# Kernel optimization log

Measured on AMD Instinct MI355X. Metric: run time of the kernel, lower is better.

## Reference

```python
import jax, jax.numpy as jnp
import numpy as np

H = 1024          # rnn hidden dim
D = H // 2        # coarse/fine half
E = H // 8        # embed dim = 128
COND = H // 2     # conditioning (upsampled mel) dim = 512
EPS = 1e-5
TILE = 16


def _bn(x, scale, offset):
    # haiku BatchNorm, training mode: batch stats over (N, L)
    mean = jnp.mean(x, axis=(0, 1), keepdims=True)
    var = jnp.mean(jnp.square(x), axis=(0, 1), keepdims=True) - jnp.square(mean)
    return scale * (x - mean) * jax.lax.rsqrt(var + EPS) + offset


def _conv(x, w, rate=1):
    return jax.lax.conv_general_dilated(
        x, w, window_strides=(1,), padding='VALID', rhs_dilation=(rate,),
        dimension_numbers=('NWC', 'WIO', 'NWC'))


def _up(x, w, stride):
    # Conv1DTranspose with kernel 1, SAME padding: scatter x@w to positions i*stride
    N, L, _ = x.shape
    y = jnp.einsum('nlc,cd->nld', x, w)
    out = jnp.zeros((N, L, stride, y.shape[-1]), y.dtype).at[:, :, 0, :].set(y)
    return out.reshape(N, L * stride, y.shape[-1])


def _iw_mask():
    m = jnp.ones((COND + 3 * E, 3 * H), jnp.float32)
    for j in (0, 2, 4):  # coarse_t embed cannot see coarse half of u, r, e gates
        m = m.at[-E:, j * D:(j + 1) * D].set(0.0)
    return m


def _forward(x, mel, conv_in_w, bn0_s, bn0_o, dconv1_w, bn1_s, bn1_o,
             dconv2_w, bn2_s, bn2_o, up1_w, bn3_s, bn3_o, up2_w, bn4_s, bn4_o,
             up3_w, bn5_s, bn5_o, I_W, I_b, R_w, R_b,
             O1_w, O1_b, O2_w, O2_b, O3_w, O3_b, O4_w, O4_b, c_embed, f_embed):
    # ---- UpsampleNetwork ----
    h = jax.nn.relu(_bn(_conv(mel, conv_in_w), bn0_s, bn0_o))
    r1 = jax.nn.relu(_bn(_conv(h, dconv1_w, rate=2), bn1_s, bn1_o))
    h = h[:, 1:-1] + r1
    r2 = jax.nn.relu(_bn(_conv(h, dconv2_w, rate=4), bn2_s, bn2_o))
    h = h[:, 2:-2] + r2
    h = jax.nn.relu(_bn(_up(h, up1_w, 2), bn3_s, bn3_o))
    h = jax.nn.relu(_bn(_up(h, up2_w, 2), bn4_s, bn4_o))
    h = jax.nn.relu(_bn(_up(h, up3_w, 4), bn5_s, bn5_o))
    N, Lm, Dm = h.shape
    mel_up = jnp.tile(h[:, :, None, :], (1, 1, TILE, 1)).reshape(N, Lm * TILE, Dm)

    # ---- WaveRNNOriginal.__call__ (teacher-forced GRU) ----
    coarse, fine, coarse_t = x[..., 0], x[..., 1], x[..., 2]
    inputs = jnp.concatenate(
        (mel_up, c_embed[coarse], f_embed[fine], c_embed[coarse_t]), axis=-1)
    # precompute input projection for all timesteps  [N, L, 3H]
    ix = jnp.einsum('nli,ij->nlj', inputs, I_W * _iw_mask()) + I_b.reshape(1, 1, -1)
    ix_t = jnp.swapaxes(ix, 0, 1)  # time-major [L, N, 3H]
    h0 = jnp.zeros((N, H), ix.dtype)

    def step(hx, xt):
        u1, r1_, e1 = jnp.split(hx @ R_w + R_b, 3, axis=-1)
        u2, r2_, e2 = jnp.split(xt, 3, axis=-1)
        ut = jax.nn.sigmoid(u1 + u2)
        rt = jax.nn.sigmoid(r1_ + r2_)
        et = jnp.tanh(rt * e1 + e2)
        ht = ut * hx + (1.0 - ut) * et
        return ht, ht

    _, hs = jax.lax.scan(step, h0, ix_t)
    hs = jnp.swapaxes(hs, 0, 1)              # [N, L, H]
    yc, yf = jnp.split(hs, 2, axis=-1)       # [N, L, H/2] each
    clog = jax.nn.relu(yc @ O1_w + O1_b) @ O2_w + O2_b
    flog = jax.nn.relu(yf @ O3_w + O3_b) @ O4_w + O4_b
    logits = jnp.stack((clog, flog), axis=-1)  # [N, L, 256, 2]
    return jax.nn.log_softmax(logits, axis=-2)


def setup_inputs():
    key = jax.random.key(0)
    ks = jax.random.split(key, 24)
    n = jax.random.normal
    N, T = 2, 24
    L = (T - 8) * 256  # 4096
    inp = {
        'x': jax.random.randint(ks[0], (N, L, 3), 0, 256),
        'mel': n(ks[1], (N, T, 80), jnp.float32),
        'conv_in_w': n(ks[2], (3, 80, 512)) * 0.05,
        'dconv1_w': n(ks[3], (2, 512, 512)) * 0.05,
        'dconv2_w': n(ks[4], (2, 512, 512)) * 0.05,
        'up1_w': n(ks[5], (512, 512)) * 0.05,
        'up2_w': n(ks[6], (512, 512)) * 0.05,
        'up3_w': n(ks[7], (512, COND)) * 0.05,
        'I_W': n(ks[8], (COND + 3 * E, 3 * H)) * 0.03,
        'I_b': jnp.zeros((3 * H,)),
        'R_w': n(ks[9], (H, 3 * H)) * 0.03,
        'R_b': jnp.zeros((3 * H,)),
        'O1_w': n(ks[10], (D, D)) * 0.05,
        'O1_b': jnp.zeros((D,)),
        'O2_w': n(ks[11], (D, 256)) * 0.05,
        'O2_b': jnp.zeros((256,)),
        'O3_w': n(ks[12], (D, D)) * 0.05,
        'O3_b': jnp.zeros((D,)),
        'O4_w': n(ks[13], (D, 256)) * 0.05,
        'O4_b': jnp.zeros((256,)),
        'c_embed': n(ks[14], (256, E)) * 0.1,
        'f_embed': n(ks[15], (256, E)) * 0.1,
    }
    for i in range(6):
        c = COND if i == 5 else 512
        inp[f'bn{i}_s'] = jnp.ones((c,))
        inp[f'bn{i}_o'] = jnp.zeros((c,))
    return inp


def reference(x, mel, conv_in_w, dconv1_w, dconv2_w, up1_w, up2_w, up3_w,
              I_W, I_b, R_w, R_b, O1_w, O1_b, O2_w, O2_b, O3_w, O3_b,
              O4_w, O4_b, c_embed, f_embed,
              bn0_s, bn0_o, bn1_s, bn1_o, bn2_s, bn2_o,
              bn3_s, bn3_o, bn4_s, bn4_o, bn5_s, bn5_o):
    return _forward(x, mel, conv_in_w, bn0_s, bn0_o, dconv1_w, bn1_s, bn1_o,
                    dconv2_w, bn2_s, bn2_o, up1_w, bn3_s, bn3_o, up2_w, bn4_s,
                    bn4_o, up3_w, bn5_s, bn5_o, I_W, I_b, R_w, R_b,
                    O1_w, O1_b, O2_w, O2_b, O3_w, O3_b, O4_w, O4_b,
                    c_embed, f_embed)
```

## Files before the change

### kernel.cpp

```cpp
#include <hip/hip_runtime.h>
#include <hip/hip_bf16.h>
#include <math.h>

__device__ __forceinline__ float bf2f(unsigned short u) {
  unsigned int x = ((unsigned int)u) << 16;
  return __builtin_bit_cast(float, x);
}
__device__ __forceinline__ unsigned short f2bf(float f) {
  unsigned int x = __builtin_bit_cast(unsigned int, f);
  unsigned int lsb = (x >> 16) & 1u;
  x += 0x7fffu + lsb;
  return (unsigned short)(x >> 16);
}
template <bool BF>
__device__ __forceinline__ float ld(const void* p, size_t i) {
  if (BF) return bf2f(((const unsigned short*)p)[i]);
  return ((const float*)p)[i];
}

#define SCOPE_AGENT __HIP_MEMORY_SCOPE_AGENT
typedef unsigned long long ull;

__global__ void k_init(const unsigned int* bn0s, ull* sbuf, int* dt) {
  int t = threadIdx.x;
  for (int i = t; i < 4096; i += 256) sbuf[i] = 0ULL;
  if (t == 0) dt[0] = (bn0s[0] == 0x3F803F80u) ? 1 : 0;
}

template <bool BF>
__device__ void conv_in_body(const void* mel, const void* w, float* out) {
  int idx = blockIdx.x * 256 + threadIdx.x;
  if (idx >= 2 * 22 * 512) return;
  int c = idx & 511, l = (idx >> 9) % 22, n = idx / (22 * 512);
  float acc = 0.f;
  for (int kw = 0; kw < 3; kw++) {
    size_t mrow = (size_t)(n * 24 + l + kw) * 80;
    size_t wrow = (size_t)kw * 80 * 512 + c;
#pragma unroll 4
    for (int i = 0; i < 80; i++)
      acc += ld<BF>(mel, mrow + i) * ld<BF>(w, wrow + (size_t)i * 512);
  }
  out[idx] = acc;
}
__global__ void k_conv_in(const void* mel, const void* w, float* out, const int* dt) {
  if (dt[0]) conv_in_body<true>(mel, w, out); else conv_in_body<false>(mel, w, out);
}

template <bool BF>
__device__ void dconv_body(const float* in, const void* w, float* out,
                           int Lin, int Lout, int rate) {
  int idx = blockIdx.x * 256 + threadIdx.x;
  if (idx >= 2 * Lout * 512) return;
  int c = idx & 511, l = (idx >> 9) % Lout, n = idx / (Lout * 512);
  float acc = 0.f;
  for (int kw = 0; kw < 2; kw++) {
    const float* irow = in + (n * Lin + l + kw * rate) * 512;
    size_t wrow = (size_t)kw * 512 * 512 + c;
#pragma unroll 4
    for (int i = 0; i < 512; i++)
      acc += irow[i] * ld<BF>(w, wrow + (size_t)i * 512);
  }
  out[idx] = acc;
}
__global__ void k_dconv(const float* in, const void* w, float* out,
                        int Lin, int Lout, int rate, const int* dt) {
  if (dt[0]) dconv_body<true>(in, w, out, Lin, Lout, rate);
  else dconv_body<false>(in, w, out, Lin, Lout, rate);
}

template <bool BF>
__device__ void up_body(const float* in, const void* w, float* out, int Lin, int stride) {
  int Lout = Lin * stride;
  int idx = blockIdx.x * 256 + threadIdx.x;
  if (idx >= 2 * Lout * 512) return;
  int c = idx & 511, lo = (idx >> 9) % Lout, n = idx / (Lout * 512);
  if (lo % stride) { out[idx] = 0.f; return; }
  const float* irow = in + (n * Lin + lo / stride) * 512;
  float acc = 0.f;
#pragma unroll 4
  for (int i = 0; i < 512; i++) acc += irow[i] * ld<BF>(w, (size_t)i * 512 + c);
  out[idx] = acc;
}
__global__ void k_up(const float* in, const void* w, float* out,
                     int Lin, int stride, const int* dt) {
  if (dt[0]) up_body<true>(in, w, out, Lin, stride);
  else up_body<false>(in, w, out, Lin, stride);
}

__global__ void k_bnstats(const float* __restrict__ x, float* __restrict__ st, int NL) {
  int c = blockIdx.x * 256 + threadIdx.x;
  if (c >= 512) return;
  float s = 0.f, s2 = 0.f;
  for (int r = 0; r < NL; r++) { float v = x[r * 512 + c]; s += v; s2 += v * v; }
  float m = s / (float)NL;
  float var = s2 / (float)NL - m * m;
  st[c] = m;
  st[512 + c] = rsqrtf(var + 1e-5f);
}

template <bool BF>
__device__ void bnrelu_body(const float* x, float* y, const float* st,
                            const void* sc, const void* of,
                            const float* res, int resL, int shift, int L) {
  int idx = blockIdx.x * 256 + threadIdx.x;
  if (idx >= 2 * L * 512) return;
  int c = idx & 511, l = (idx >> 9) % L, n = idx / (L * 512);
  float v = (x[idx] - st[c]) * st[512 + c] * ld<BF>(sc, c) + ld<BF>(of, c);
  v = fmaxf(v, 0.f);
  if (res) v += res[(n * resL + l + shift) * 512 + c];
  y[idx] = v;
}
__global__ void k_bnrelu(const float* x, float* y, const float* st,
                         const void* sc, const void* of,
                         const float* res, int resL, int shift, int L, const int* dt) {
  if (dt[0]) bnrelu_body<true>(x, y, st, sc, of, res, resL, shift, L);
  else bnrelu_body<false>(x, y, st, sc, of, res, resL, shift, L);
}

template <bool BF>
__device__ void M_body(const float* h5, const void* IW, const void* Ib,
                       const void* Rb, float* M) {
  int bid = blockIdx.x;
  int row = bid / 12;
  int j = (bid % 12) * 256 + threadIdx.x;
  const float* h = h5 + row * 512;
  float acc = 0.f;
#pragma unroll 8
  for (int k = 0; k < 512; k++) acc += h[k] * ld<BF>(IW, (size_t)k * 3072 + j);
  acc += ld<BF>(Ib, j);
  if (j < 2048) acc += ld<BF>(Rb, j);
  M[(size_t)row * 3072 + j] = acc;
}
__global__ void k_M(const float* h5, const void* IW, const void* Ib,
                    const void* Rb, float* M, const int* dt) {
  if (dt[0]) M_body<true>(h5, IW, Ib, Rb, M); else M_body<false>(h5, IW, Ib, Rb, M);
}

template <bool BF>
__device__ void T_body(const void* emb, const void* IW, int row0, int maskcoarse,
                       float* T) {
  int bid = blockIdx.x;
  int v = bid / 12;
  int j = (bid % 12) * 256 + threadIdx.x;
  float acc = 0.f;
#pragma unroll 8
  for (int k = 0; k < 128; k++)
    acc += ld<BF>(emb, (size_t)v * 128 + k) *
           ld<BF>(IW, (size_t)(row0 + k) * 3072 + j);
  if (maskcoarse && ((j & 1023) < 512)) acc = 0.f;
  T[(size_t)v * 3072 + j] = acc;
}
__global__ void k_T(const void* emb, const void* IW, int row0, int maskcoarse,
                    float* T, const int* dt) {
  if (dt[0]) T_body<true>(emb, IW, row0, maskcoarse, T);
  else T_body<false>(emb, IW, row0, maskcoarse, T);
}

#define NWG 128
template <bool BF>
__device__ void gru_body(const float* __restrict__ M, const float* __restrict__ T1,
                         const float* __restrict__ T2, const float* __restrict__ T3,
                         const int* __restrict__ x, const void* Rw, const void* Rb,
                         ull* sbuf, unsigned short* __restrict__ hs, float* hlds) {
  const int g = blockIdx.x, tid = threadIdx.x;
  const int n = g >> 6;
  const int il = tid >> 4, ks = tid & 15;
  const int i = (g & 63) * 16 + il;
  const int koff = ks * 64;
  const int k0 = tid * 4;
  const int lidx = (k0 >> 6) * 68 + (k0 & 63);

  float wreg[192];
#pragma unroll
  for (int gt = 0; gt < 3; gt++)
#pragma unroll
    for (int kk = 0; kk < 64; kk++)
      wreg[gt * 64 + kk] = ld<BF>(Rw, (size_t)(koff + kk) * 3072 + gt * 1024 + i);
  const float rbe = ld<BF>(Rb, 2048 + i);

  float hprev = 0.f;

  for (int t = 0; t < 4096; t++) {
    float au = 0.f, ar = 0.f, ae = 0.f;
    if (ks == 0) {
      const int* xr = x + (n * 4096 + t) * 3;
      int ci = xr[0], fi = xr[1], cti = xr[2];
      const float* mr = M + (size_t)(n * 256 + (t >> 4)) * 3072;
      const float* p1 = T1 + (size_t)ci * 3072;
      const float* p2 = T2 + (size_t)fi * 3072;
      const float* p3 = T3 + (size_t)cti * 3072;
      au = mr[i] + p1[i] + p2[i] + p3[i];
      ar = mr[1024 + i] + p1[1024 + i] + p2[1024 + i] + p3[1024 + i];
      ae = mr[2048 + i] + p1[2048 + i] + p2[2048 + i] + p3[2048 + i];
    }

    ull* sb = sbuf + (size_t)(((t & 1) << 1) + n) * 1024 + k0;
    ull s0, s1, s2, s3;
    while (true) {
      s0 = __hip_atomic_load(sb + 0, __ATOMIC_RELAXED, SCOPE_AGENT);
      s1 = __hip_atomic_load(sb + 1, __ATOMIC_RELAXED, SCOPE_AGENT);
      s2 = __hip_atomic_load(sb + 2, __ATOMIC_RELAXED, SCOPE_AGENT);
      s3 = __hip_atomic_load(sb + 3, __ATOMIC_RELAXED, SCOPE_AGENT);
      unsigned int t0 = (unsigned int)(s0 >> 32), t1 = (unsigned int)(s1 >> 32);
      unsigned int t2 = (unsigned int)(s2 >> 32), t3 = (unsigned int)(s3 >> 32);
      if (t0 >= (unsigned)t && t1 >= (unsigned)t && t2 >= (unsigned)t &&
          t3 >= (unsigned)t) break;
      __builtin_amdgcn_s_sleep(1);
    }
    float4 h4s;
    h4s.x = __builtin_bit_cast(float, (unsigned int)s0);
    h4s.y = __builtin_bit_cast(float, (unsigned int)s1);
    h4s.z = __builtin_bit_cast(float, (unsigned int)s2);
    h4s.w = __builtin_bit_cast(float, (unsigned int)s3);
    *(float4*)(hlds + lidx) = h4s;
    __syncthreads();

    float du = 0.f, dr = 0.f, de = 0.f;
    const float* hp = hlds + ks * 68;
#pragma unroll
    for (int kk = 0; kk < 64; kk += 4) {
      float4 h4 = *(const float4*)(hp + kk);
      du += wreg[kk] * h4.x + wreg[kk + 1] * h4.y + wreg[kk + 2] * h4.z + wreg[kk + 3] * h4.w;
      dr += wreg[64 + kk] * h4.x + wreg[65 + kk] * h4.y + wreg[66 + kk] * h4.z + wreg[67 + kk] * h4.w;
      de += wreg[128 + kk] * h4.x + wreg[129 + kk] * h4.y + wreg[130 + kk] * h4.z + wreg[131 + kk] * h4.w;
    }
#pragma unroll
    for (int off = 8; off > 0; off >>= 1) {
      du += __shfl_xor(du, off, 16);
      dr += __shfl_xor(dr, off, 16);
      de += __shfl_xor(de, off, 16);
    }

    if (ks == 0) {
      float u = 1.f / (1.f + __expf(-(du + au)));
      float r = 1.f / (1.f + __expf(-(dr + ar)));
      float e = tanhf(r * (de + rbe) + ae);
      float ht = u * hprev + (1.f - u) * e;
      hprev = ht;
      ull slot = ((ull)(unsigned int)(t + 1) << 32) |
                 (ull)__builtin_bit_cast(unsigned int, ht);
      __hip_atomic_store(
          sbuf + (size_t)((((t + 1) & 1) << 1) + n) * 1024 + i, slot,
          __ATOMIC_RELAXED, SCOPE_AGENT);
      hs[(size_t)(n * 4096 + t) * 1024 + i] = f2bf(ht);
    }
  }
}
__global__ __launch_bounds__(256, 1) void k_gru(
    const float* M, const float* T1, const float* T2, const float* T3,
    const int* x, const void* Rw, const void* Rb,
    ull* sbuf, unsigned short* hs, const int* dt) {
  __shared__ float hlds[16 * 68];
  if (dt[0]) gru_body<true>(M, T1, T2, T3, x, Rw, Rb, sbuf, hs, hlds);
  else gru_body<false>(M, T1, T2, T3, x, Rw, Rb, sbuf, hs, hlds);
}

template <bool BF>
__device__ void out1_body(const unsigned short* __restrict__ hs,
                          const void* O1w, const void* O1b,
                          const void* O3w, const void* O3b,
                          unsigned short* __restrict__ tmid, unsigned short* lds) {
  int b = blockIdx.x, tid = threadIdx.x;
  size_t r0 = (size_t)b * 16;
  const uint4* src = (const uint4*)(hs + r0 * 1024);
  uint4* dst = (uint4*)lds;
  for (int q = tid; q < 2048; q += 256) dst[q] = src[q];
  __syncthreads();

  float acc[4][16];
#pragma unroll
  for (int jg = 0; jg < 4; jg++)
#pragma unroll
    for (int r = 0; r < 16; r++) acc[jg][r] = 0.f;

  for (int k = 0; k < 512; k++) {
    float w0 = ld<BF>(O1w, (size_t)k * 512 + tid);
    float w1 = ld<BF>(O1w, (size_t)k * 512 + 256 + tid);
    float w2 = ld<BF>(O3w, (size_t)k * 512 + tid);
    float w3 = ld<BF>(O3w, (size_t)k * 512 + 256 + tid);
#pragma unroll
    for (int r = 0; r < 16; r++) {
      float hc = bf2f(lds[r * 1024 + k]);
      float hf = bf2f(lds[r * 1024 + 512 + k]);
      acc[0][r] += hc * w0; acc[1][r] += hc * w1;
      acc[2][r] += hf * w2; acc[3][r] += hf * w3;
    }
  }
  float bia[4] = { ld<BF>(O1b, tid), ld<BF>(O1b, 256 + tid),
                   ld<BF>(O3b, tid), ld<BF>(O3b, 256 + tid) };
#pragma unroll
  for (int jg = 0; jg < 4; jg++)
#pragma unroll
    for (int r = 0; r < 16; r++) {
      float v = fmaxf(acc[jg][r] + bia[jg], 0.f);
      tmid[(r0 + r) * 1024 + jg * 256 + tid] = f2bf(v);
    }
}
__global__ __launch_bounds__(256) void k_out1(
    const unsigned short* hs, const void* O1w, const void* O1b,
    const void* O3w, const void* O3b, unsigned short* tmid, const int* dt) {
  __shared__ unsigned short lds[16 * 1024];
  if (dt[0]) out1_body<true>(hs, O1w, O1b, O3w, O3b, tmid, lds);
  else out1_body<false>(hs, O1w, O1b, O3w, O3b, tmid, lds);
}

__device__ __forceinline__ float blkmax(float v, float* red, int tid) {
#pragma unroll
  for (int off = 32; off > 0; off >>= 1) v = fmaxf(v, __shfl_xor(v, off));
  __syncthreads();
  if ((tid & 63) == 0) red[tid >> 6] = v;
  __syncthreads();
  return fmaxf(fmaxf(red[0], red[1]), fmaxf(red[2], red[3]));
}
__device__ __forceinline__ float blksum(float v, float* red, int tid) {
#pragma unroll
  for (int off = 32; off > 0; off >>= 1) v += __shfl_xor(v, off);
  __syncthreads();
  if ((tid & 63) == 0) red[tid >> 6] = v;
  __syncthreads();
  return red[0] + red[1] + red[2] + red[3];
}

template <bool BF>
__device__ void out2_body(const unsigned short* __restrict__ tmid,
                          const void* O2w, const void* O2b,
                          const void* O4w, const void* O4b,
                          void* out, unsigned short* lds, float* red) {
  int b = blockIdx.x, tid = threadIdx.x, q = tid;
  size_t r0 = (size_t)b * 16;
  const uint4* src = (const uint4*)(tmid + r0 * 1024);
  uint4* dst = (uint4*)lds;
  for (int p = tid; p < 2048; p += 256) dst[p] = src[p];
  __syncthreads();

  float ac[16], af[16];
#pragma unroll
  for (int r = 0; r < 16; r++) { ac[r] = 0.f; af[r] = 0.f; }
  for (int j = 0; j < 512; j++) {
    float w2 = ld<BF>(O2w, (size_t)j * 256 + q);
    float w4 = ld<BF>(O4w, (size_t)j * 256 + q);
#pragma unroll
    for (int r = 0; r < 16; r++) {
      ac[r] += bf2f(lds[r * 1024 + j]) * w2;
      af[r] += bf2f(lds[r * 1024 + 512 + j]) * w4;
    }
  }
  float b2 = ld<BF>(O2b, q), b4 = ld<BF>(O4b, q);
  for (int r = 0; r < 16; r++) {
    float c = ac[r] + b2;
    float f = af[r] + b4;
    float mc = blkmax(c, red, tid);
    float sc = blksum(__expf(c - mc), red, tid);
    float mf = blkmax(f, red, tid);
    float sf = blksum(__expf(f - mf), red, tid);
    size_t row = r0 + r;
    float oc = c - mc - logf(sc);
    float of_ = f - mf - logf(sf);
    if (BF) {
      ((unsigned short*)out)[(row * 256 + q) * 2 + 0] = f2bf(oc);
      ((unsigned short*)out)[(row * 256 + q) * 2 + 1] = f2bf(of_);
    } else {
      ((float*)out)[(row * 256 + q) * 2 + 0] = oc;
      ((float*)out)[(row * 256 + q) * 2 + 1] = of_;
    }
  }
}
__global__ __launch_bounds__(256) void k_out2(
    const unsigned short* tmid, const void* O2w, const void* O2b,
    const void* O4w, const void* O4b, void* out, const int* dt) {
  __shared__ unsigned short lds[16 * 1024];
  __shared__ float red[8];
  if (dt[0]) out2_body<true>(tmid, O2w, O2b, O4w, O4b, out, lds, red);
  else out2_body<false>(tmid, O2w, O2b, O4w, O4b, out, lds, red);
}

extern "C" void kernel_launch(void* const* d_in, const int* in_sizes, int n_in,
                              void* d_out, int out_size, void* d_ws, size_t ws_size,
                              hipStream_t stream) {
  const int* x = (const int*)d_in[0];
  const void* mel = d_in[1];
  const void* conv_in_w = d_in[2];
  const void* dconv1_w = d_in[3];
  const void* dconv2_w = d_in[4];
  const void* up1_w = d_in[5];
  const void* up2_w = d_in[6];
  const void* up3_w = d_in[7];
  const void* IW = d_in[8];
  const void* Ib = d_in[9];
  const void* Rw = d_in[10];
  const void* Rb = d_in[11];
  const void* O1w = d_in[12];
  const void* O1b = d_in[13];
  const void* O2w = d_in[14];
  const void* O2b = d_in[15];
  const void* O3w = d_in[16];
  const void* O3b = d_in[17];
  const void* O4w = d_in[18];
  const void* O4b = d_in[19];
  const void* c_embed = d_in[20];
  const void* f_embed = d_in[21];
  const void* bns[6], *bno[6];
  for (int s = 0; s < 6; s++) {
    bns[s] = d_in[22 + 2 * s];
    bno[s] = d_in[23 + 2 * s];
  }

  float* ws = (float*)d_ws;
  float* A = ws;
  float* B = A + 262144;
  float* st = B + 262144;
  float* M = st + 1024;
  float* T1 = M + 1572864;
  float* T2 = T1 + 786432;
  float* T3 = T2 + 786432;
  ull* sbuf = (ull*)(T3 + 786432);
  int* dt = (int*)(sbuf + 4096);
  unsigned short* hs = (unsigned short*)(dt + 4);
  unsigned short* tmid = hs + 8388608;

  k_init<<<1, 256, 0, stream>>>((const unsigned int*)bns[0], sbuf, dt);

  k_conv_in<<<88, 256, 0, stream>>>(mel, conv_in_w, A, dt);
  k_bnstats<<<2, 256, 0, stream>>>(A, st, 44);
  k_bnrelu<<<88, 256, 0, stream>>>(A, A, st, bns[0], bno[0], nullptr, 0, 0, 22, dt);

  k_dconv<<<80, 256, 0, stream>>>(A, dconv1_w, B, 22, 20, 2, dt);
  k_bnstats<<<2, 256, 0, stream>>>(B, st, 40);
  k_bnrelu<<<80, 256, 0, stream>>>(B, B, st, bns[1], bno[1], A, 22, 1, 20, dt);

  k_dconv<<<64, 256, 0, stream>>>(B, dconv2_w, A, 20, 16, 4, dt);
  k_bnstats<<<2, 256, 0, stream>>>(A, st, 32);
  k_bnrelu<<<64, 256, 0, stream>>>(A, A, st, bns[2], bno[2], B, 20, 2, 16, dt);

  k_up<<<128, 256, 0, stream>>>(A, up1_w, B, 16, 2, dt);
  k_bnstats<<<2, 256, 0, stream>>>(B, st, 64);
  k_bnrelu<<<128, 256, 0, stream>>>(B, B, st, bns[3], bno[3], nullptr, 0, 0, 32, dt);

  k_up<<<256, 256, 0, stream>>>(B, up2_w, A, 32, 2, dt);
  k_bnstats<<<2, 256, 0, stream>>>(A, st, 128);
  k_bnrelu<<<256, 256, 0, stream>>>(A, A, st, bns[4], bno[4], nullptr, 0, 0, 64, dt);

  k_up<<<1024, 256, 0, stream>>>(A, up3_w, B, 64, 4, dt);
  k_bnstats<<<2, 256, 0, stream>>>(B, st, 512);
  k_bnrelu<<<1024, 256, 0, stream>>>(B, B, st, bns[5], bno[5], nullptr, 0, 0, 256, dt);

  k_M<<<6144, 256, 0, stream>>>(B, IW, Ib, Rb, M, dt);
  k_T<<<3072, 256, 0, stream>>>(c_embed, IW, 512, 0, T1, dt);
  k_T<<<3072, 256, 0, stream>>>(f_embed, IW, 640, 0, T2, dt);
  k_T<<<3072, 256, 0, stream>>>(c_embed, IW, 768, 1, T3, dt);

  k_gru<<<NWG, 256, 0, stream>>>(M, T1, T2, T3, x, Rw, Rb, sbuf, hs, dt);

  k_out1<<<512, 256, 0, stream>>>(hs, O1w, O1b, O3w, O3b, tmid, dt);
  k_out2<<<512, 256, 0, stream>>>(tmid, O2w, O2b, O4w, O4b, d_out, dt);

  (void)in_sizes; (void)n_in; (void)out_size; (void)ws_size;
}
```

Before: 10.10 ms.

## Widen GRU workgroups to 512 threads and tile M/T precompute over rows

The GRU recurrence kernel now runs 512 threads per workgroup, and each lane covers 32 of the hidden dimension instead of 64. This halves the per-thread register weights and shortens the serial dot-product chain in each timestep. The spin-wait drops the sleep and compares packed 64-bit values directly, tanh becomes an exp-based form, and a second barrier per step guards the shared buffer. The M and T precompute kernels now stage 8 input rows in LDS, so each weight load is reused across 8 outputs. Trade-offs are extra barrier cost per step, busier polling of the atomic flags, and a slightly less accurate tanh.

```diff
diff --git a/kernel.cpp b/kernel.cpp
--- a/kernel.cpp
+++ b/kernel.cpp
@@ -119,41 +119,73 @@
 
 template <bool BF>
 __device__ void M_body(const float* h5, const void* IW, const void* Ib,
-                       const void* Rb, float* M) {
+                       const void* Rb, float* M, float* hl) {
   int bid = blockIdx.x;
-  int row = bid / 12;
-  int j = (bid % 12) * 256 + threadIdx.x;
-  const float* h = h5 + row * 512;
-  float acc = 0.f;
-#pragma unroll 8
-  for (int k = 0; k < 512; k++) acc += h[k] * ld<BF>(IW, (size_t)k * 3072 + j);
-  acc += ld<BF>(Ib, j);
-  if (j < 2048) acc += ld<BF>(Rb, j);
-  M[(size_t)row * 3072 + j] = acc;
-}
-__global__ void k_M(const float* h5, const void* IW, const void* Ib,
-                    const void* Rb, float* M, const int* dt) {
-  if (dt[0]) M_body<true>(h5, IW, Ib, Rb, M); else M_body<false>(h5, IW, Ib, Rb, M);
+  int rt = bid / 12, ct = bid % 12;
+  int r0 = rt * 8, j = ct * 256 + threadIdx.x;
+  const float4* src = (const float4*)(h5 + (size_t)r0 * 512);
+  float4* dst = (float4*)hl;
+  for (int q = threadIdx.x; q < 1024; q += 256) dst[q] = src[q];
+  __syncthreads();
+  float acc[8];
+#pragma unroll
+  for (int r = 0; r < 8; r++) acc[r] = 0.f;
+  for (int k = 0; k < 512; k += 4) {
+    float w0 = ld<BF>(IW, (size_t)k * 3072 + j);
+    float w1 = ld<BF>(IW, (size_t)(k + 1) * 3072 + j);
+    float w2 = ld<BF>(IW, (size_t)(k + 2) * 3072 + j);
+    float w3 = ld<BF>(IW, (size_t)(k + 3) * 3072 + j);
+#pragma unroll
+    for (int r = 0; r < 8; r++) {
+      float4 h4 = *(const float4*)(hl + r * 512 + k);
+      acc[r] += h4.x * w0 + h4.y * w1 + h4.z * w2 + h4.w * w3;
+    }
+  }
+  float bias = ld<BF>(Ib, j) + ((j < 2048) ? ld<BF>(Rb, j) : 0.f);
+#pragma unroll
+  for (int r = 0; r < 8; r++) M[(size_t)(r0 + r) * 3072 + j] = acc[r] + bias;
+}
+__global__ __launch_bounds__(256) void k_M(const float* h5, const void* IW,
+                                           const void* Ib, const void* Rb,
+                                           float* M, const int* dt) {
+  __shared__ float hl[8 * 512];
+  if (dt[0]) M_body<true>(h5, IW, Ib, Rb, M, hl);
+  else M_body<false>(h5, IW, Ib, Rb, M, hl);
 }
 
 template <bool BF>
 __device__ void T_body(const void* emb, const void* IW, int row0, int maskcoarse,
-                       float* T) {
+                       float* T, float* el) {
   int bid = blockIdx.x;
-  int v = bid / 12;
-  int j = (bid % 12) * 256 + threadIdx.x;
-  float acc = 0.f;
-#pragma unroll 8
-  for (int k = 0; k < 128; k++)
-    acc += ld<BF>(emb, (size_t)v * 128 + k) *
-           ld<BF>(IW, (size_t)(row0 + k) * 3072 + j);
-  if (maskcoarse && ((j & 1023) < 512)) acc = 0.f;
-  T[(size_t)v * 3072 + j] = acc;
-}
-__global__ void k_T(const void* emb, const void* IW, int row0, int maskcoarse,
-                    float* T, const int* dt) {
-  if (dt[0]) T_body<true>(emb, IW, row0, maskcoarse, T);
-  else T_body<false>(emb, IW, row0, maskcoarse, T);
+  int vt = bid / 12, ct = bid % 12;
+  int v0 = vt * 8, j = ct * 256 + threadIdx.x;
+  for (int q = threadIdx.x; q < 1024; q += 256)
+    el[q] = ld<BF>(emb, (size_t)v0 * 128 + q);
+  __syncthreads();
+  float acc[8];
+#pragma unroll
+  for (int r = 0; r < 8; r++) acc[r] = 0.f;
+  for (int k = 0; k < 128; k += 4) {
+    float w0 = ld<BF>(IW, (size_t)(row0 + k) * 3072 + j);
+    float w1 = ld<BF>(IW, (size_t)(row0 + k + 1) * 3072 + j);
+    float w2 = ld<BF>(IW, (size_t)(row0 + k + 2) * 3072 + j);
+    float w3 = ld<BF>(IW, (size_t)(row0 + k + 3) * 3072 + j);
+#pragma unroll
+    for (int r = 0; r < 8; r++) {
+      float4 e4 = *(const float4*)(el + r * 128 + k);
+      acc[r] += e4.x * w0 + e4.y * w1 + e4.z * w2 + e4.w * w3;
+    }
+  }
+  bool mask = maskcoarse && ((j & 1023) < 512);
+#pragma unroll
+  for (int r = 0; r < 8; r++)
+    T[(size_t)(v0 + r) * 3072 + j] = mask ? 0.f : acc[r];
+}
+__global__ __launch_bounds__(256) void k_T(const void* emb, const void* IW, int row0,
+                                           int maskcoarse, float* T, const int* dt) {
+  __shared__ float el[8 * 128];
+  if (dt[0]) T_body<true>(emb, IW, row0, maskcoarse, T, el);
+  else T_body<false>(emb, IW, row0, maskcoarse, T, el);
 }
 
 #define NWG 128
@@ -164,18 +196,18 @@
                          ull* sbuf, unsigned short* __restrict__ hs, float* hlds) {
   const int g = blockIdx.x, tid = threadIdx.x;
   const int n = g >> 6;
-  const int il = tid >> 4, ks = tid & 15;
+  const int il = tid >> 5, ks = tid & 31;
   const int i = (g & 63) * 16 + il;
-  const int koff = ks * 64;
-  const int k0 = tid * 4;
+  const int koff = ks * 32;
+  const int k0 = tid * 2;
   const int lidx = (k0 >> 6) * 68 + (k0 & 63);
 
-  float wreg[192];
+  float wreg[96];
 #pragma unroll
   for (int gt = 0; gt < 3; gt++)
 #pragma unroll
-    for (int kk = 0; kk < 64; kk++)
-      wreg[gt * 64 + kk] = ld<BF>(Rw, (size_t)(koff + kk) * 3072 + gt * 1024 + i);
+    for (int kk = 0; kk < 32; kk++)
+      wreg[gt * 32 + kk] = ld<BF>(Rw, (size_t)(koff + kk) * 3072 + gt * 1024 + i);
   const float rbe = ld<BF>(Rb, 2048 + i);
 
   float hprev = 0.f;
@@ -194,47 +226,41 @@
       ae = mr[2048 + i] + p1[2048 + i] + p2[2048 + i] + p3[2048 + i];
     }
 
+    const ull thr = (ull)(unsigned int)t << 32;
     ull* sb = sbuf + (size_t)(((t & 1) << 1) + n) * 1024 + k0;
-    ull s0, s1, s2, s3;
+    ull s0, s1;
     while (true) {
       s0 = __hip_atomic_load(sb + 0, __ATOMIC_RELAXED, SCOPE_AGENT);
       s1 = __hip_atomic_load(sb + 1, __ATOMIC_RELAXED, SCOPE_AGENT);
-      s2 = __hip_atomic_load(sb + 2, __ATOMIC_RELAXED, SCOPE_AGENT);
-      s3 = __hip_atomic_load(sb + 3, __ATOMIC_RELAXED, SCOPE_AGENT);
-      unsigned int t0 = (unsigned int)(s0 >> 32), t1 = (unsigned int)(s1 >> 32);
-      unsigned int t2 = (unsigned int)(s2 >> 32), t3 = (unsigned int)(s3 >> 32);
-      if (t0 >= (unsigned)t && t1 >= (unsigned)t && t2 >= (unsigned)t &&
-          t3 >= (unsigned)t) break;
-      __builtin_amdgcn_s_sleep(1);
-    }
-    float4 h4s;
-    h4s.x = __builtin_bit_cast(float, (unsigned int)s0);
-    h4s.y = __builtin_bit_cast(float, (unsigned int)s1);
-    h4s.z = __builtin_bit_cast(float, (unsigned int)s2);
-    h4s.w = __builtin_bit_cast(float, (unsigned int)s3);
-    *(float4*)(hlds + lidx) = h4s;
+      if (s0 >= thr && s1 >= thr) break;
+    }
+    float2 h2;
+    h2.x = __builtin_bit_cast(float, (unsigned int)s0);
+    h2.y = __builtin_bit_cast(float, (unsigned int)s1);
+    *(float2*)(hlds + lidx) = h2;
     __syncthreads();
 
     float du = 0.f, dr = 0.f, de = 0.f;
-    const float* hp = hlds + ks * 68;
-#pragma unroll
-    for (int kk = 0; kk < 64; kk += 4) {
+    const float* hp = hlds + (ks >> 1) * 68 + (ks & 1) * 32;
+#pragma unroll
+    for (int kk = 0; kk < 32; kk += 4) {
       float4 h4 = *(const float4*)(hp + kk);
       du += wreg[kk] * h4.x + wreg[kk + 1] * h4.y + wreg[kk + 2] * h4.z + wreg[kk + 3] * h4.w;
-      dr += wreg[64 + kk] * h4.x + wreg[65 + kk] * h4.y + wreg[66 + kk] * h4.z + wreg[67 + kk] * h4.w;
-      de += wreg[128 + kk] * h4.x + wreg[129 + kk] * h4.y + wreg[130 + kk] * h4.z + wreg[131 + kk] * h4.w;
-    }
-#pragma unroll
-    for (int off = 8; off > 0; off >>= 1) {
-      du += __shfl_xor(du, off, 16);
-      dr += __shfl_xor(dr, off, 16);
-      de += __shfl_xor(de, off, 16);
+      dr += wreg[32 + kk] * h4.x + wreg[33 + kk] * h4.y + wreg[34 + kk] * h4.z + wreg[35 + kk] * h4.w;
+      de += wreg[64 + kk] * h4.x + wreg[65 + kk] * h4.y + wreg[66 + kk] * h4.z + wreg[67 + kk] * h4.w;
+    }
+#pragma unroll
+    for (int off = 16; off > 0; off >>= 1) {
+      du += __shfl_xor(du, off, 32);
+      dr += __shfl_xor(dr, off, 32);
+      de += __shfl_xor(de, off, 32);
     }
 
     if (ks == 0) {
       float u = 1.f / (1.f + __expf(-(du + au)));
       float r = 1.f / (1.f + __expf(-(dr + ar)));
-      float e = tanhf(r * (de + rbe) + ae);
+      float w = r * (de + rbe) + ae;
+      float e = 1.f - 2.f / (__expf(2.f * w) + 1.f);
       float ht = u * hprev + (1.f - u) * e;
       hprev = ht;
       ull slot = ((ull)(unsigned int)(t + 1) << 32) |
@@ -244,13 +270,14 @@
           __ATOMIC_RELAXED, SCOPE_AGENT);
       hs[(size_t)(n * 4096 + t) * 1024 + i] = f2bf(ht);
     }
-  }
-}
-__global__ __launch_bounds__(256, 1) void k_gru(
+    __syncthreads();
+  }
+}
+__global__ __launch_bounds__(512, 1) void k_gru(
     const float* M, const float* T1, const float* T2, const float* T3,
     const int* x, const void* Rw, const void* Rb,
     ull* sbuf, unsigned short* hs, const int* dt) {
-  __shared__ float hlds[16 * 68];
+  __shared__ __align__(16) float hlds[16 * 68];
   if (dt[0]) gru_body<true>(M, T1, T2, T3, x, Rw, Rb, sbuf, hs, hlds);
   else gru_body<false>(M, T1, T2, T3, x, Rw, Rb, sbuf, hs, hlds);
 }
@@ -444,12 +471,12 @@
   k_bnstats<<<2, 256, 0, stream>>>(B, st, 512);
   k_bnrelu<<<1024, 256, 0, stream>>>(B, B, st, bns[5], bno[5], nullptr, 0, 0, 256, dt);
 
-  k_M<<<6144, 256, 0, stream>>>(B, IW, Ib, Rb, M, dt);
-  k_T<<<3072, 256, 0, stream>>>(c_embed, IW, 512, 0, T1, dt);
-  k_T<<<3072, 256, 0, stream>>>(f_embed, IW, 640, 0, T2, dt);
-  k_T<<<3072, 256, 0, stream>>>(c_embed, IW, 768, 1, T3, dt);
-
-  k_gru<<<NWG, 256, 0, stream>>>(M, T1, T2, T3, x, Rw, Rb, sbuf, hs, dt);
+  k_M<<<768, 256, 0, stream>>>(B, IW, Ib, Rb, M, dt);
+  k_T<<<384, 256, 0, stream>>>(c_embed, IW, 512, 0, T1, dt);
+  k_T<<<384, 256, 0, stream>>>(f_embed, IW, 640, 0, T2, dt);
+  k_T<<<384, 256, 0, stream>>>(c_embed, IW, 768, 1, T3, dt);
+
+  k_gru<<<NWG, 512, 0, stream>>>(M, T1, T2, T3, x, Rw, Rb, sbuf, hs, dt);
 
   k_out1<<<512, 256, 0, stream>>>(hs, O1w, O1b, O3w, O3b, tmid, dt);
   k_out2<<<512, 256, 0, stream>>>(tmid, O2w, O2b, O4w, O4b, d_out, dt);
```

Measured after the change: 9.246 ms. 1.09x faster.
